# Performance work log

Measured on AMD Instinct MI355X. Metric: run time of the kernel, lower is better.

Reference implementation:

```python
import jax, jax.numpy as jnp
import numpy as np

N_NODES = 40000
N_EDGES = 640000
HIDDEN = 128


def setup_inputs() -> dict:
    key = jax.random.key(0)
    k_h, k_w, k_b, k_src, k_dst = jax.random.split(key, 5)
    h = jax.random.normal(k_h, (N_NODES, HIDDEN), dtype=jnp.float32)
    # nn.Linear(hidden_dim, hidden_dim): weight [out, in], bias [out]
    W = jax.random.normal(k_w, (HIDDEN, HIDDEN), dtype=jnp.float32) * (1.0 / np.sqrt(HIDDEN))
    b = jax.random.normal(k_b, (HIDDEN,), dtype=jnp.float32) * 0.01
    src = jax.random.randint(k_src, (N_EDGES,), 0, N_NODES, dtype=jnp.int32)
    dst = jax.random.randint(k_dst, (N_EDGES,), 0, N_NODES, dtype=jnp.int32)
    return {"h": h, "W": W, "b": b, "src": src, "dst": dst}


def reference(h, W, b, src, dst):
    n = h.shape[0]
    # message: gather source node features; reduce: mailbox sum == segment-sum by dst
    agg = jax.ops.segment_sum(h[src], dst, num_segments=n)  # [N, D]
    updated = agg @ W.T + b  # merge_linner
    # DGL update_all only writes nodes with >=1 incoming edge; others keep old h
    indeg = jax.ops.segment_sum(jnp.ones(src.shape, dtype=h.dtype), dst, num_segments=n)
    return jnp.where((indeg > 0)[:, None], updated, h)
```

## Files before the change

kernel.cpp:

```cpp
#include <hip/hip_runtime.h>
#include <hip/hip_bf16.h>

static constexpr int HIDDEN = 128;

using bf16x8 = __attribute__((ext_vector_type(8))) __bf16;
using f32x4 = __attribute__((ext_vector_type(4))) float;
using ushort8v = __attribute__((ext_vector_type(8))) ushort;

__device__ inline ushort f2bf(float x) {
  __hip_bfloat16 t = __float2bfloat16(x);
  return *reinterpret_cast<ushort*>(&t);
}

__global__ void __launch_bounds__(256) hist_wconv_kernel(
    const int* __restrict__ dst, int* __restrict__ counts, int n_edges,
    int nbh, const float* __restrict__ W, ushort* __restrict__ wbf) {
  if (blockIdx.x < nbh) {
    int i = (blockIdx.x * 256 + threadIdx.x) * 4;
    if (i + 3 < n_edges) {
      int4 d = *reinterpret_cast<const int4*>(dst + i);
      atomicAdd(&counts[d.x], 1);
      atomicAdd(&counts[d.y], 1);
      atomicAdd(&counts[d.z], 1);
      atomicAdd(&counts[d.w], 1);
    } else {
      for (int j = i; j < n_edges; ++j) atomicAdd(&counts[dst[j]], 1);
    }
  } else {
    int i = ((blockIdx.x - nbh) * 256 + threadIdx.x) * 4;
    if (i < HIDDEN * HIDDEN) {
      float4 w = *reinterpret_cast<const float4*>(W + i);
      ushort4 u;
      u.x = f2bf(w.x);
      u.y = f2bf(w.y);
      u.z = f2bf(w.z);
      u.w = f2bf(w.w);
      *reinterpret_cast<ushort4*>(wbf + i) = u;
    }
  }
}

__global__ void __launch_bounds__(256) scanA_kernel(
    const int* __restrict__ counts, int* __restrict__ tilesums, int n) {
  const int t = threadIdx.x;
  const int base = blockIdx.x * 1024 + t * 4;
  int s = 0;
  if (base + 3 < n) {
    int4 v = *reinterpret_cast<const int4*>(counts + base);
    s = v.x + v.y + v.z + v.w;
  } else {
    for (int j = 0; j < 4; ++j)
      if (base + j < n) s += counts[base + j];
  }
  for (int off = 1; off < 64; off <<= 1) s += __shfl_xor(s, off, 64);
  __shared__ int wp[4];
  if ((t & 63) == 0) wp[t >> 6] = s;
  __syncthreads();
  if (t == 0) tilesums[blockIdx.x] = wp[0] + wp[1] + wp[2] + wp[3];
}

__global__ void __launch_bounds__(256) scanC_kernel(
    const int* __restrict__ counts, const int* __restrict__ tilesums,
    int* __restrict__ offsets, int n, int nt) {
  __shared__ int tp[64];
  const int t = threadIdx.x;
  if (t < 64) {
    int v = (t < nt) ? tilesums[t] : 0;
    int orig = v;
    for (int off = 1; off < 64; off <<= 1) {
      int u = __shfl_up(v, off, 64);
      if (t >= off) v += u;
    }
    tp[t] = v - orig;
  }
  __syncthreads();

  const int base = blockIdx.x * 1024 + t * 4;
  int4 v = {0, 0, 0, 0};
  const bool full = (base + 3 < n);
  if (full) {
    v = *reinterpret_cast<const int4*>(counts + base);
  } else {
    if (base + 0 < n) v.x = counts[base + 0];
    if (base + 1 < n) v.y = counts[base + 1];
    if (base + 2 < n) v.z = counts[base + 2];
    if (base + 3 < n) v.w = counts[base + 3];
  }
  const int s = v.x + v.y + v.z + v.w;
  int inc = s;
  for (int off = 1; off < 64; off <<= 1) {
    int u = __shfl_up(inc, off, 64);
    if ((t & 63) >= off) inc += u;
  }
  const int excl = inc - s;
  __shared__ int wp[4];
  if ((t & 63) == 63) wp[t >> 6] = inc;
  __syncthreads();
  int wbase = 0;
  for (int w = 0; w < (t >> 6); ++w) wbase += wp[w];
  int p = tp[blockIdx.x] + wbase + excl;
  if (full) {
    int4 o;
    o.x = p;
    o.y = p + v.x;
    o.z = p + v.x + v.y;
    o.w = p + v.x + v.y + v.z;
    *reinterpret_cast<int4*>(offsets + base) = o;
  } else {
    int run = p;
    if (base + 0 < n) { offsets[base + 0] = run; run += v.x; }
    if (base + 1 < n) { offsets[base + 1] = run; run += v.y; }
    if (base + 2 < n) { offsets[base + 2] = run; run += v.z; }
    if (base + 3 < n) { offsets[base + 3] = run; }
  }
}

__global__ void __launch_bounds__(256) fill_kernel(
    const int* __restrict__ src, const int* __restrict__ dst,
    int* __restrict__ offsets, int* __restrict__ esorted, int n_edges) {
  int i = (blockIdx.x * 256 + threadIdx.x) * 4;
  if (i + 3 < n_edges) {
    int4 s = *reinterpret_cast<const int4*>(src + i);
    int4 d = *reinterpret_cast<const int4*>(dst + i);
    int p0 = atomicAdd(&offsets[d.x], 1);
    int p1 = atomicAdd(&offsets[d.y], 1);
    int p2 = atomicAdd(&offsets[d.z], 1);
    int p3 = atomicAdd(&offsets[d.w], 1);
    esorted[p0] = s.x;
    esorted[p1] = s.y;
    esorted[p2] = s.z;
    esorted[p3] = s.w;
  } else {
    for (int j = i; j < n_edges; ++j) {
      int pos = atomicAdd(&offsets[dst[j]], 1);
      esorted[pos] = src[j];
    }
  }
}

__global__ void __launch_bounds__(256) transform_mfma_kernel(
    const float* __restrict__ h, const ushort* __restrict__ wbf,
    ushort* __restrict__ hW, int n_nodes) {
  constexpr int COLP = 136;
  __shared__ ushort tile[4][16][COLP];
  const int wave = threadIdx.x >> 6;
  const int lane = threadIdx.x & 63;
  const int r16 = lane & 15;
  const int kq = lane >> 4;
  const int kbase = kq * 8;
  const int base = blockIdx.x * 64 + wave * 16;

  int arow = base + r16;
  if (arow >= n_nodes) arow = n_nodes - 1;
  const float* hrow = h + (size_t)arow * HIDDEN;

  bf16x8 a[4];
#pragma unroll
  for (int ks = 0; ks < 4; ++ks) {
    const float4 u = *reinterpret_cast<const float4*>(hrow + ks * 32 + kbase);
    const float4 v =
        *reinterpret_cast<const float4*>(hrow + ks * 32 + kbase + 4);
    bf16x8 t;
    t[0] = (__bf16)u.x;
    t[1] = (__bf16)u.y;
    t[2] = (__bf16)u.z;
    t[3] = (__bf16)u.w;
    t[4] = (__bf16)v.x;
    t[5] = (__bf16)v.y;
    t[6] = (__bf16)v.z;
    t[7] = (__bf16)v.w;
    a[ks] = t;
  }

#pragma unroll
  for (int ct = 0; ct < 8; ++ct) {
    const ushort* wrow = wbf + (size_t)(ct * 16 + r16) * HIDDEN;
    f32x4 acc = {0.f, 0.f, 0.f, 0.f};
#pragma unroll
    for (int ks = 0; ks < 4; ++ks) {
      bf16x8 bfrag = *reinterpret_cast<const bf16x8*>(wrow + ks * 32 + kbase);
      acc = __builtin_amdgcn_mfma_f32_16x16x32_bf16(a[ks], bfrag, acc, 0, 0, 0);
    }
#pragma unroll
    for (int r = 0; r < 4; ++r)
      tile[wave][kq * 4 + r][ct * 16 + r16] = f2bf(acc[r]);
  }
#pragma unroll
  for (int it = 0; it < 4; ++it) {
    const int row = it * 4 + (lane >> 4);
    const int cb = r16 * 8;
    const int nrow = base + row;
    if (nrow < n_nodes) {
      ushort8v v = *reinterpret_cast<const ushort8v*>(&tile[wave][row][cb]);
      *reinterpret_cast<ushort8v*>(hW + (size_t)nrow * HIDDEN + cb) = v;
    }
  }
}

__global__ void __launch_bounds__(256) gather_sum_kernel(
    const ushort* __restrict__ hW, const float* __restrict__ h,
    const float* __restrict__ b, const int* __restrict__ counts,
    const int* __restrict__ ends, const int* __restrict__ esorted,
    float* __restrict__ out, int n_nodes) {
  const int lane = threadIdx.x & 15;
  const int group = threadIdx.x >> 4;
  const int f0 = lane * 8;
  const int node = blockIdx.x * 16 + group;
  if (node >= n_nodes) return;

  const int deg = counts[node];
  f32x4 o0, o1;
  if (deg == 0) {
    float4 t0 = *reinterpret_cast<const float4*>(h + (size_t)node * HIDDEN + f0);
    float4 t1 =
        *reinterpret_cast<const float4*>(h + (size_t)node * HIDDEN + f0 + 4);
    o0 = {t0.x, t0.y, t0.z, t0.w};
    o1 = {t1.x, t1.y, t1.z, t1.w};
  } else {
    const int start = ends[node] - deg;
    float4 A = {0.f, 0.f, 0.f, 0.f};
    float4 B = {0.f, 0.f, 0.f, 0.f};
    for (int base = 0; base < deg; base += 16) {
      int sreg = 0;
      if (base + lane < deg)
        sreg = __builtin_nontemporal_load(esorted + start + base + lane);
      const int m = min(16, deg - base);
#pragma unroll 8
      for (int jj = 0; jj < m; ++jj) {
        int s = __shfl(sreg, jj, 16);
        uint4 v = *reinterpret_cast<const uint4*>(hW + (size_t)s * HIDDEN + f0);
        A.x += __uint_as_float(v.x << 16);
        A.y += __uint_as_float(v.x & 0xffff0000u);
        A.z += __uint_as_float(v.y << 16);
        A.w += __uint_as_float(v.y & 0xffff0000u);
        B.x += __uint_as_float(v.z << 16);
        B.y += __uint_as_float(v.z & 0xffff0000u);
        B.z += __uint_as_float(v.w << 16);
        B.w += __uint_as_float(v.w & 0xffff0000u);
      }
    }
    const float4 b0 = *reinterpret_cast<const float4*>(b + f0);
    const float4 b1 = *reinterpret_cast<const float4*>(b + f0 + 4);
    o0 = {A.x + b0.x, A.y + b0.y, A.z + b0.z, A.w + b0.w};
    o1 = {B.x + b1.x, B.y + b1.y, B.z + b1.z, B.w + b1.w};
  }
  __builtin_nontemporal_store(
      o0, reinterpret_cast<f32x4*>(out + (size_t)node * HIDDEN + f0));
  __builtin_nontemporal_store(
      o1, reinterpret_cast<f32x4*>(out + (size_t)node * HIDDEN + f0 + 4));
}


__global__ void __launch_bounds__(256) hist_kernel(
    const int* __restrict__ dst, int* __restrict__ counts, int n_edges) {
  int i = blockIdx.x * 256 + threadIdx.x;
  if (i < n_edges) atomicAdd(&counts[dst[i]], 1);
}

__global__ void __launch_bounds__(256) fill1_kernel(
    const int* __restrict__ src, const int* __restrict__ dst,
    int* __restrict__ offsets, int* __restrict__ esorted, int n_edges) {
  int i = blockIdx.x * 256 + threadIdx.x;
  if (i < n_edges) {
    int pos = atomicAdd(&offsets[dst[i]], 1);
    esorted[pos] = src[i];
  }
}

__global__ void __launch_bounds__(1024) scan_kernel(
    const int* __restrict__ counts, int* __restrict__ offsets, int n) {
  __shared__ int part[1024];
  const int t = threadIdx.x;
  const int C = (n + 1023) / 1024;
  const int base = t * C;
  int sum = 0;
  for (int j = 0; j < C; ++j) {
    int idx = base + j;
    if (idx < n) sum += counts[idx];
  }
  part[t] = sum;
  __syncthreads();
  for (int s = 1; s < 1024; s <<= 1) {
    int v = (t >= s) ? part[t - s] : 0;
    __syncthreads();
    part[t] += v;
    __syncthreads();
  }
  int run = part[t] - sum;
  for (int j = 0; j < C; ++j) {
    int idx = base + j;
    if (idx < n) {
      offsets[idx] = run;
      run += counts[idx];
    }
  }
}

__global__ void __launch_bounds__(256, 2) gather_update_kernel(
    const float* __restrict__ h, const float* __restrict__ W,
    const float* __restrict__ b, const int* __restrict__ counts,
    const int* __restrict__ ends, const int* __restrict__ esorted,
    float* __restrict__ out, int n_nodes) {
  __shared__ float Wt[HIDDEN][HIDDEN];
  for (int i = threadIdx.x; i < HIDDEN * HIDDEN / 4; i += 256) {
    int idx = i * 4;
    int j = idx >> 7;
    int k = idx & 127;
    float4 w = *reinterpret_cast<const float4*>(W + j * HIDDEN + k);
    Wt[k + 0][j] = w.x;
    Wt[k + 1][j] = w.y;
    Wt[k + 2][j] = w.z;
    Wt[k + 3][j] = w.w;
  }
  __syncthreads();
  const int lane = threadIdx.x & 31;
  const int group = threadIdx.x >> 5;
  const int j0 = lane * 4;
  const float4 bias = *reinterpret_cast<const float4*>(b + j0);
  const int nb = (n_nodes + 7) >> 3;
  for (int batch = blockIdx.x; batch < nb; batch += gridDim.x) {
    int node = batch * 8 + group;
    if (node >= n_nodes) continue;
    const int deg = counts[node];
    float4 res;
    if (deg == 0) {
      res = reinterpret_cast<const float4*>(h + (size_t)node * HIDDEN)[lane];
    } else {
      const int start = ends[node] - deg;
      float4 acc = {0.f, 0.f, 0.f, 0.f};
      for (int basei = 0; basei < deg; basei += 32) {
        int sreg = 0;
        if (basei + lane < deg) sreg = esorted[start + basei + lane];
        const int m = min(32, deg - basei);
        for (int jj = 0; jj < m; ++jj) {
          int s = __shfl(sreg, jj, 32);
          float4 v =
              reinterpret_cast<const float4*>(h + (size_t)s * HIDDEN)[lane];
          acc.x += v.x;
          acc.y += v.y;
          acc.z += v.z;
          acc.w += v.w;
        }
      }
      const float* av = reinterpret_cast<const float*>(&acc);
      float4 o = bias;
#pragma unroll
      for (int k = 0; k < HIDDEN; ++k) {
        float aval = __shfl(av[k & 3], k >> 2, 32);
        float4 w = *reinterpret_cast<const float4*>(&Wt[k][j0]);
        o.x = fmaf(aval, w.x, o.x);
        o.y = fmaf(aval, w.y, o.y);
        o.z = fmaf(aval, w.z, o.z);
        o.w = fmaf(aval, w.w, o.w);
      }
      res = o;
    }
    reinterpret_cast<float4*>(out + (size_t)node * HIDDEN)[lane] = res;
  }
}


extern "C" void kernel_launch(void* const* d_in, const int* in_sizes, int n_in,
                              void* d_out, int out_size, void* d_ws, size_t ws_size,
                              hipStream_t stream) {
  const float* h = (const float*)d_in[0];
  const float* W = (const float*)d_in[1];
  const float* b = (const float*)d_in[2];
  const int* src = (const int*)d_in[3];
  const int* dst = (const int*)d_in[4];
  float* out = (float*)d_out;
  const int n_nodes = in_sizes[0] / HIDDEN;
  const int n_edges = in_sizes[3];

  const int n_round = (n_nodes + 1023) & ~1023;
  const int nt = n_round / 1024;
  const int eblocks4 = (n_edges + 1023) / 1024;

  int* counts = (int*)d_ws;
  int* offsets = counts + n_round;
  int* tilesums = offsets + n_round;
  int* esorted = tilesums + 64;
  size_t off_bytes = ((size_t)(2 * n_round + 64 + n_edges) * 4 + 15) & ~15ull;
  ushort* hW = (ushort*)((char*)d_ws + off_bytes);
  size_t wbf_off = (off_bytes + (size_t)n_nodes * HIDDEN * 2 + 15) & ~15ull;
  ushort* wbf = (ushort*)((char*)d_ws + wbf_off);
  const size_t need_full = wbf_off + (size_t)HIDDEN * HIDDEN * 2;

  if (ws_size >= need_full && nt <= 64) {
    (void)hipMemsetAsync(counts, 0, (size_t)n_nodes * sizeof(int), stream);
    const int wblocks = (HIDDEN * HIDDEN + 1023) / 1024;
    hist_wconv_kernel<<<eblocks4 + wblocks, 256, 0, stream>>>(
        dst, counts, n_edges, eblocks4, W, wbf);
    scanA_kernel<<<nt, 256, 0, stream>>>(counts, tilesums, n_nodes);
    scanC_kernel<<<nt, 256, 0, stream>>>(counts, tilesums, offsets, n_nodes,
                                         nt);
    fill_kernel<<<eblocks4, 256, 0, stream>>>(src, dst, offsets, esorted,
                                              n_edges);
    const int tblocks = (n_nodes + 63) / 64;
    transform_mfma_kernel<<<tblocks, 256, 0, stream>>>(h, wbf, hW, n_nodes);
    const int gblocks = (n_nodes + 15) / 16;
    gather_sum_kernel<<<gblocks, 256, 0, stream>>>(hW, h, b, counts, offsets,
                                                   esorted, out, n_nodes);
  } else {
    (void)hipMemsetAsync(counts, 0, (size_t)n_nodes * sizeof(int), stream);
    const int eblocks = (n_edges + 255) / 256;
    hist_kernel<<<eblocks, 256, 0, stream>>>(dst, counts, n_edges);
    scan_kernel<<<1, 1024, 0, stream>>>(counts, offsets, n_nodes);
    fill1_kernel<<<eblocks, 256, 0, stream>>>(src, dst, offsets, esorted,
                                              n_edges);
    gather_update_kernel<<<512, 256, 0, stream>>>(h, W, b, counts, offsets,
                                                  esorted, out, n_nodes);
  }
}
```

Baseline: 184.0 us.

## Fuse edge fill with MFMA transform and widen per-lane gather width

The edge-sorting fill kernel and the MFMA feature-transform kernel are merged into one launch, with each block picking its role from its block index, so the two independent stages overlap and one launch is saved. The gather kernel now uses 8 lanes per node, each handling 16 features through two 16-byte loads, and a block covers 32 nodes instead of 16. This gives more memory parallelism per lane and fewer shuffles per edge, at the cost of more registers per thread. Fill blocks also reserve the transform kernel's shared memory, which could lower occupancy.

```diff
diff --git a/kernel.cpp b/kernel.cpp
--- a/kernel.cpp
+++ b/kernel.cpp
@@ -115,40 +115,43 @@
   }
 }
 
-__global__ void __launch_bounds__(256) fill_kernel(
+__global__ void __launch_bounds__(256) fill_transform_kernel(
     const int* __restrict__ src, const int* __restrict__ dst,
-    int* __restrict__ offsets, int* __restrict__ esorted, int n_edges) {
-  int i = (blockIdx.x * 256 + threadIdx.x) * 4;
-  if (i + 3 < n_edges) {
-    int4 s = *reinterpret_cast<const int4*>(src + i);
-    int4 d = *reinterpret_cast<const int4*>(dst + i);
-    int p0 = atomicAdd(&offsets[d.x], 1);
-    int p1 = atomicAdd(&offsets[d.y], 1);
-    int p2 = atomicAdd(&offsets[d.z], 1);
-    int p3 = atomicAdd(&offsets[d.w], 1);
-    esorted[p0] = s.x;
-    esorted[p1] = s.y;
-    esorted[p2] = s.z;
-    esorted[p3] = s.w;
-  } else {
-    for (int j = i; j < n_edges; ++j) {
-      int pos = atomicAdd(&offsets[dst[j]], 1);
-      esorted[pos] = src[j];
-    }
-  }
-}
-
-__global__ void __launch_bounds__(256) transform_mfma_kernel(
-    const float* __restrict__ h, const ushort* __restrict__ wbf,
+    int* __restrict__ offsets, int* __restrict__ esorted, int n_edges,
+    int nbf, const float* __restrict__ h, const ushort* __restrict__ wbf,
     ushort* __restrict__ hW, int n_nodes) {
   constexpr int COLP = 136;
   __shared__ ushort tile[4][16][COLP];
+
+  if (blockIdx.x < nbf) {
+    int i = (blockIdx.x * 256 + threadIdx.x) * 4;
+    if (i + 3 < n_edges) {
+      int4 s = *reinterpret_cast<const int4*>(src + i);
+      int4 d = *reinterpret_cast<const int4*>(dst + i);
+      int p0 = atomicAdd(&offsets[d.x], 1);
+      int p1 = atomicAdd(&offsets[d.y], 1);
+      int p2 = atomicAdd(&offsets[d.z], 1);
+      int p3 = atomicAdd(&offsets[d.w], 1);
+      esorted[p0] = s.x;
+      esorted[p1] = s.y;
+      esorted[p2] = s.z;
+      esorted[p3] = s.w;
+    } else {
+      for (int j = i; j < n_edges; ++j) {
+        int pos = atomicAdd(&offsets[dst[j]], 1);
+        esorted[pos] = src[j];
+      }
+    }
+    return;
+  }
+
+  const int tb = blockIdx.x - nbf;
   const int wave = threadIdx.x >> 6;
   const int lane = threadIdx.x & 63;
   const int r16 = lane & 15;
   const int kq = lane >> 4;
   const int kbase = kq * 8;
-  const int base = blockIdx.x * 64 + wave * 16;
+  const int base = tb * 64 + wave * 16;
 
   int arow = base + r16;
   if (arow >= n_nodes) arow = n_nodes - 1;
@@ -202,52 +205,73 @@
     const float* __restrict__ b, const int* __restrict__ counts,
     const int* __restrict__ ends, const int* __restrict__ esorted,
     float* __restrict__ out, int n_nodes) {
-  const int lane = threadIdx.x & 15;
-  const int group = threadIdx.x >> 4;
-  const int f0 = lane * 8;
-  const int node = blockIdx.x * 16 + group;
+  const int lane = threadIdx.x & 7;
+  const int group = threadIdx.x >> 3;
+  const int f0 = lane * 16;
+  const int node = blockIdx.x * 32 + group;
   if (node >= n_nodes) return;
 
   const int deg = counts[node];
-  f32x4 o0, o1;
+  f32x4 A = {0.f, 0.f, 0.f, 0.f};
+  f32x4 B = {0.f, 0.f, 0.f, 0.f};
+  f32x4 C = {0.f, 0.f, 0.f, 0.f};
+  f32x4 D = {0.f, 0.f, 0.f, 0.f};
   if (deg == 0) {
-    float4 t0 = *reinterpret_cast<const float4*>(h + (size_t)node * HIDDEN + f0);
-    float4 t1 =
-        *reinterpret_cast<const float4*>(h + (size_t)node * HIDDEN + f0 + 4);
-    o0 = {t0.x, t0.y, t0.z, t0.w};
-    o1 = {t1.x, t1.y, t1.z, t1.w};
+    const float* hr = h + (size_t)node * HIDDEN + f0;
+    float4 t0 = *reinterpret_cast<const float4*>(hr + 0);
+    float4 t1 = *reinterpret_cast<const float4*>(hr + 4);
+    float4 t2 = *reinterpret_cast<const float4*>(hr + 8);
+    float4 t3 = *reinterpret_cast<const float4*>(hr + 12);
+    A = {t0.x, t0.y, t0.z, t0.w};
+    B = {t1.x, t1.y, t1.z, t1.w};
+    C = {t2.x, t2.y, t2.z, t2.w};
+    D = {t3.x, t3.y, t3.z, t3.w};
   } else {
     const int start = ends[node] - deg;
-    float4 A = {0.f, 0.f, 0.f, 0.f};
-    float4 B = {0.f, 0.f, 0.f, 0.f};
-    for (int base = 0; base < deg; base += 16) {
+    for (int base = 0; base < deg; base += 8) {
       int sreg = 0;
       if (base + lane < deg)
         sreg = __builtin_nontemporal_load(esorted + start + base + lane);
-      const int m = min(16, deg - base);
+      const int m = min(8, deg - base);
 #pragma unroll 8
       for (int jj = 0; jj < m; ++jj) {
-        int s = __shfl(sreg, jj, 16);
-        uint4 v = *reinterpret_cast<const uint4*>(hW + (size_t)s * HIDDEN + f0);
-        A.x += __uint_as_float(v.x << 16);
-        A.y += __uint_as_float(v.x & 0xffff0000u);
-        A.z += __uint_as_float(v.y << 16);
-        A.w += __uint_as_float(v.y & 0xffff0000u);
-        B.x += __uint_as_float(v.z << 16);
-        B.y += __uint_as_float(v.z & 0xffff0000u);
-        B.z += __uint_as_float(v.w << 16);
-        B.w += __uint_as_float(v.w & 0xffff0000u);
+        int s = __shfl(sreg, jj, 8);
+        const uint4* rp =
+            reinterpret_cast<const uint4*>(hW + (size_t)s * HIDDEN + f0);
+        uint4 v0 = rp[0];
+        uint4 v1 = rp[1];
+        A[0] += __uint_as_float(v0.x << 16);
+        A[1] += __uint_as_float(v0.x & 0xffff0000u);
+        A[2] += __uint_as_float(v0.y << 16);
+        A[3] += __uint_as_float(v0.y & 0xffff0000u);
+        B[0] += __uint_as_float(v0.z << 16);
+        B[1] += __uint_as_float(v0.z & 0xffff0000u);
+        B[2] += __uint_as_float(v0.w << 16);
+        B[3] += __uint_as_float(v0.w & 0xffff0000u);
+        C[0] += __uint_as_float(v1.x << 16);
+        C[1] += __uint_as_float(v1.x & 0xffff0000u);
+        C[2] += __uint_as_float(v1.y << 16);
+        C[3] += __uint_as_float(v1.y & 0xffff0000u);
+        D[0] += __uint_as_float(v1.z << 16);
+        D[1] += __uint_as_float(v1.z & 0xffff0000u);
+        D[2] += __uint_as_float(v1.w << 16);
+        D[3] += __uint_as_float(v1.w & 0xffff0000u);
       }
     }
-    const float4 b0 = *reinterpret_cast<const float4*>(b + f0);
+    const float4 b0 = *reinterpret_cast<const float4*>(b + f0 + 0);
     const float4 b1 = *reinterpret_cast<const float4*>(b + f0 + 4);
-    o0 = {A.x + b0.x, A.y + b0.y, A.z + b0.z, A.w + b0.w};
-    o1 = {B.x + b1.x, B.y + b1.y, B.z + b1.z, B.w + b1.w};
-  }
-  __builtin_nontemporal_store(
-      o0, reinterpret_cast<f32x4*>(out + (size_t)node * HIDDEN + f0));
-  __builtin_nontemporal_store(
-      o1, reinterpret_cast<f32x4*>(out + (size_t)node * HIDDEN + f0 + 4));
+    const float4 b2 = *reinterpret_cast<const float4*>(b + f0 + 8);
+    const float4 b3 = *reinterpret_cast<const float4*>(b + f0 + 12);
+    A[0] += b0.x; A[1] += b0.y; A[2] += b0.z; A[3] += b0.w;
+    B[0] += b1.x; B[1] += b1.y; B[2] += b1.z; B[3] += b1.w;
+    C[0] += b2.x; C[1] += b2.y; C[2] += b2.z; C[3] += b2.w;
+    D[0] += b3.x; D[1] += b3.y; D[2] += b3.z; D[3] += b3.w;
+  }
+  float* op = out + (size_t)node * HIDDEN + f0;
+  __builtin_nontemporal_store(A, reinterpret_cast<f32x4*>(op + 0));
+  __builtin_nontemporal_store(B, reinterpret_cast<f32x4*>(op + 4));
+  __builtin_nontemporal_store(C, reinterpret_cast<f32x4*>(op + 8));
+  __builtin_nontemporal_store(D, reinterpret_cast<f32x4*>(op + 12));
 }
 
 
@@ -394,11 +418,10 @@
     scanA_kernel<<<nt, 256, 0, stream>>>(counts, tilesums, n_nodes);
     scanC_kernel<<<nt, 256, 0, stream>>>(counts, tilesums, offsets, n_nodes,
                                          nt);
-    fill_kernel<<<eblocks4, 256, 0, stream>>>(src, dst, offsets, esorted,
-                                              n_edges);
     const int tblocks = (n_nodes + 63) / 64;
-    transform_mfma_kernel<<<tblocks, 256, 0, stream>>>(h, wbf, hW, n_nodes);
-    const int gblocks = (n_nodes + 15) / 16;
+    fill_transform_kernel<<<eblocks4 + tblocks, 256, 0, stream>>>(
+        src, dst, offsets, esorted, n_edges, eblocks4, h, wbf, hW, n_nodes);
+    const int gblocks = (n_nodes + 31) / 32;
     gather_sum_kernel<<<gblocks, 256, 0, stream>>>(hW, h, b, counts, offsets,
                                                    esorted, out, n_nodes);
   } else {
```

New measurement: 177.8 us. 1.04x faster.
